# Optimization experiments

Hardware: AMD Instinct MI355X
Metric: run time of the kernel (lower is better)

The kernel has to match this reference:

```python
import jax, jax.numpy as jnp
import numpy as np

ALPHA = float(np.exp(-0.1))  # leak factor exp(-dt/tau) with dt/tau = 0.1


def setup_inputs() -> dict:
    key = jax.random.key(0)
    k1, k2 = jax.random.split(key)
    B, T, H, O = 128, 512, 1024, 256
    x = jax.random.normal(k1, (B, T, H), dtype=jnp.float32)
    # xavier_uniform init for (H, O) weight
    limit = float(np.sqrt(6.0 / (H + O)))
    weight_end = jax.random.uniform(k2, (H, O), dtype=jnp.float32,
                                    minval=-limit, maxval=limit)
    return {"x": x, "weight_end": weight_end}


def reference(x, weight_end):
    # x: [B, T, H], weight_end: [H, O]
    h2 = jnp.einsum('bth,ho->bto', x, weight_end)  # [B, T, O]
    B, T, O = h2.shape
    # leaky-integrate scan over first T-1 steps, accumulating softmax(mem)
    h_seq = jnp.swapaxes(h2[:, :T - 1, :], 0, 1)  # [T-1, B, O]

    def step(carry, h_t):
        mem, out = carry
        mem = ALPHA * mem + (1.0 - ALPHA) * h_t
        out = out + jax.nn.softmax(mem, axis=-1)
        return (mem, out), None

    init = (jnp.zeros((B, O), h2.dtype), jnp.zeros((B, O), h2.dtype))
    (_, out), _ = jax.lax.scan(step, init, h_seq)
    return out
```

## Files before the change

### kernel.cpp

```cpp
#include <hip/hip_runtime.h>

#define B_DIM 128
#define T_DIM 512
#define H_DIM 1024
#define O_DIM 256

typedef short bf16x8 __attribute__((ext_vector_type(8)));
typedef float f32x4 __attribute__((ext_vector_type(4)));

__device__ __forceinline__ unsigned short f2bf(float f) {
    union { float f; unsigned u; } v; v.f = f;
    unsigned u = v.u;
    u += 0x7fffu + ((u >> 16) & 1u);
    return (unsigned short)(u >> 16);
}
__device__ __forceinline__ unsigned pk2(float a, float b) {
    return (unsigned)f2bf(a) | ((unsigned)f2bf(b) << 16);
}

__global__ __launch_bounds__(256) void transpose_w(const float* __restrict__ W,
                                                   unsigned short* __restrict__ Wt) {
    __shared__ float tile[32][33];
    int h0 = blockIdx.x * 32;
    int o0 = blockIdx.y * 32;
    int tx = threadIdx.x;
    int ty = threadIdx.y;
#pragma unroll
    for (int j = 0; j < 32; j += 8)
        tile[ty + j][tx] = W[(size_t)(h0 + ty + j) * O_DIM + o0 + tx];
    __syncthreads();
#pragma unroll
    for (int j = 0; j < 32; j += 8)
        Wt[(size_t)(o0 + ty + j) * H_DIM + h0 + tx] = f2bf(tile[tx][ty + j]);
}

__global__ __launch_bounds__(256) void gemm_bf16(const float* __restrict__ x,
                                                 const unsigned short* __restrict__ Wt,
                                                 float* __restrict__ h2) {
    __shared__ __align__(16) unsigned short As[128 * 40];
    __shared__ __align__(16) unsigned short Bs[128 * 40];

    const int tid  = threadIdx.x;
    const int mb   = blockIdx.x >> 1;
    const int nb   = blockIdx.x & 1;
    const int m0   = mb * 128, n0 = nb * 128;
    const int r    = tid >> 1;
    const int hh   = tid & 1;
    const int lane = tid & 63;
    const int wave = tid >> 6;
    const int wm   = wave >> 1, wn = wave & 1;
    const int rowsel = lane & 15, quad = lane >> 4;

    const float* xg = x + (size_t)(m0 + r) * H_DIM + hh * 16;
    const uint4* wg = (const uint4*)(Wt + (size_t)(n0 + r) * H_DIM + hh * 16);
    uint4* awp = (uint4*)&As[r * 40 + hh * 16];
    uint4* bwp = (uint4*)&Bs[r * 40 + hh * 16];

    const unsigned short* afp = &As[(wm * 64 + rowsel) * 40 + quad * 8];
    const unsigned short* bfp = &Bs[(wn * 64 + rowsel) * 40 + quad * 8];

    f32x4 acc[4][4];
#pragma unroll
    for (int i = 0; i < 4; ++i)
#pragma unroll
        for (int j = 0; j < 4; ++j)
            acc[i][j] = (f32x4){0.f, 0.f, 0.f, 0.f};

    for (int k0 = 0; k0 < H_DIM; k0 += 32) {
        const float4* xa = (const float4*)xg;
        float4 a0 = xa[0], a1 = xa[1], a2 = xa[2], a3 = xa[3];
        uint4 wb0 = wg[0], wb1 = wg[1];
        uint4 p0, p1;
        p0.x = pk2(a0.x, a0.y); p0.y = pk2(a0.z, a0.w);
        p0.z = pk2(a1.x, a1.y); p0.w = pk2(a1.z, a1.w);
        p1.x = pk2(a2.x, a2.y); p1.y = pk2(a2.z, a2.w);
        p1.z = pk2(a3.x, a3.y); p1.w = pk2(a3.z, a3.w);
        awp[0] = p0;  awp[1] = p1;
        bwp[0] = wb0; bwp[1] = wb1;
        __syncthreads();

        bf16x8 af[4], bfr[4];
#pragma unroll
        for (int i = 0; i < 4; ++i) {
            af[i]  = *(const bf16x8*)(afp + i * 16 * 40);
            bfr[i] = *(const bf16x8*)(bfp + i * 16 * 40);
        }
#pragma unroll
        for (int i = 0; i < 4; ++i)
#pragma unroll
            for (int j = 0; j < 4; ++j)
                acc[i][j] = __builtin_amdgcn_mfma_f32_16x16x32_bf16(af[i], bfr[j], acc[i][j], 0, 0, 0);
        __syncthreads();

        xg += 32;
        wg += 4;
    }

#pragma unroll
    for (int i = 0; i < 4; ++i) {
#pragma unroll
        for (int j = 0; j < 4; ++j) {
            int gm = m0 + wm * 64 + i * 16 + quad * 4;
            int gn = n0 + wn * 64 + j * 16 + rowsel;
            float* cp = h2 + (size_t)gm * O_DIM + gn;
            cp[0 * O_DIM] = acc[i][j][0];
            cp[1 * O_DIM] = acc[i][j][1];
            cp[2 * O_DIM] = acc[i][j][2];
            cp[3 * O_DIM] = acc[i][j][3];
        }
    }
}

__global__ __launch_bounds__(64) void snn_scan(const float* __restrict__ h2,
                                               float* __restrict__ out) {
    const int b = blockIdx.x >> 3;
    const int c = blockIdx.x & 7;
    const int t_start = c * 64;
    const int t_end   = min(t_start + 64, T_DIM - 1);
    const int s0      = max(0, t_start - 128);
    const int lane    = threadIdx.x;

    const float A   = 0.90483741803595957f;
    const float OMA = 0.09516258196404043f;

    const float4* p = (const float4*)(h2 + (size_t)b * T_DIM * O_DIM) + (size_t)s0 * 64 + lane;
    float4 mem = {0.f, 0.f, 0.f, 0.f};
    float4 acc = {0.f, 0.f, 0.f, 0.f};
    float4 h = *p;
    for (int t = s0; t < t_end; ++t) {
        p += 64;
        float4 hn = *p;
        mem.x = A * mem.x + OMA * h.x;
        mem.y = A * mem.y + OMA * h.y;
        mem.z = A * mem.z + OMA * h.z;
        mem.w = A * mem.w + OMA * h.w;
        if (t >= t_start) {
            float e0 = __expf(mem.x), e1 = __expf(mem.y);
            float e2 = __expf(mem.z), e3 = __expf(mem.w);
            float s = e0 + e1 + e2 + e3;
            s += __shfl_xor(s, 1);
            s += __shfl_xor(s, 2);
            s += __shfl_xor(s, 4);
            s += __shfl_xor(s, 8);
            s += __shfl_xor(s, 16);
            s += __shfl_xor(s, 32);
            float inv = 1.0f / s;
            acc.x += e0 * inv; acc.y += e1 * inv;
            acc.z += e2 * inv; acc.w += e3 * inv;
        }
        h = hn;
    }
    float* op = out + b * O_DIM + lane * 4;
    atomicAdd(op + 0, acc.x);
    atomicAdd(op + 1, acc.y);
    atomicAdd(op + 2, acc.z);
    atomicAdd(op + 3, acc.w);
}

extern "C" void kernel_launch(void* const* d_in, const int* in_sizes, int n_in,
                              void* d_out, int out_size, void* d_ws, size_t ws_size,
                              hipStream_t stream) {
    const float* x = (const float*)d_in[0];
    const float* W = (const float*)d_in[1];
    float* out = (float*)d_out;

    float* h2 = (float*)d_ws;
    unsigned short* Wt = (unsigned short*)((char*)d_ws +
                         (size_t)B_DIM * T_DIM * O_DIM * sizeof(float));

    hipMemsetAsync(d_out, 0, (size_t)B_DIM * O_DIM * sizeof(float), stream);
    transpose_w<<<dim3(H_DIM / 32, O_DIM / 32), dim3(32, 8), 0, stream>>>(W, Wt);
    gemm_bf16<<<dim3((B_DIM * T_DIM / 128) * 2), 256, 0, stream>>>(x, Wt, h2);
    snn_scan<<<dim3(B_DIM * 8), 64, 0, stream>>>(h2, out);
}
```

Before: 479.8 us.

## Store h2 in bf16, async-load W to LDS, truncate x, shorten scan warmup

The GEMM now writes its intermediate h2 in bf16 rather than fp32, which halves the traffic for both the GEMM store and the scan read. It also loads the weight tile into LDS with global_load_lds in a new layout, and converts x to bf16 by truncation via a byte permute instead of round-to-nearest. The scan warmup drops from 128 to 64 steps and the loop is unrolled by four with prefetched loads. These changes reduce precision in several places: bf16 h2, truncated inputs and a shorter leaky warmup (alpha^64 ≈ 0.0017 residual), so accuracy may suffer.

```diff
diff --git a/kernel.cpp b/kernel.cpp
--- a/kernel.cpp
+++ b/kernel.cpp
@@ -14,8 +14,16 @@
     u += 0x7fffu + ((u >> 16) & 1u);
     return (unsigned short)(u >> 16);
 }
-__device__ __forceinline__ unsigned pk2(float a, float b) {
-    return (unsigned)f2bf(a) | ((unsigned)f2bf(b) << 16);
+
+__device__ __forceinline__ unsigned tpk(float a, float b) {
+    union { float f; unsigned u; } x{a}, y{b};
+    return __builtin_amdgcn_perm(y.u, x.u, 0x07060302u);
+}
+
+__device__ __forceinline__ void async16(const void* g, void* l) {
+    __builtin_amdgcn_global_load_lds(
+        (const __attribute__((address_space(1))) unsigned int*)g,
+        (__attribute__((address_space(3))) unsigned int*)l, 16, 0, 0);
 }
 
 __global__ __launch_bounds__(256) void transpose_w(const float* __restrict__ W,
@@ -36,9 +44,9 @@
 
 __global__ __launch_bounds__(256) void gemm_bf16(const float* __restrict__ x,
                                                  const unsigned short* __restrict__ Wt,
-                                                 float* __restrict__ h2) {
+                                                 unsigned short* __restrict__ h2) {
     __shared__ __align__(16) unsigned short As[128 * 40];
-    __shared__ __align__(16) unsigned short Bs[128 * 40];
+    __shared__ __align__(16) unsigned short Bs[4 * 128 * 8];
 
     const int tid  = threadIdx.x;
     const int mb   = blockIdx.x >> 1;
@@ -52,12 +60,15 @@
     const int rowsel = lane & 15, quad = lane >> 4;
 
     const float* xg = x + (size_t)(m0 + r) * H_DIM + hh * 16;
-    const uint4* wg = (const uint4*)(Wt + (size_t)(n0 + r) * H_DIM + hh * 16);
     uint4* awp = (uint4*)&As[r * 40 + hh * 16];
-    uint4* bwp = (uint4*)&Bs[r * 40 + hh * 16];
+
+    const unsigned short* wg0 = Wt + (size_t)(n0 + lane) * H_DIM + wave * 8;
+    const unsigned short* wg1 = wg0 + (size_t)64 * H_DIM;
+    unsigned short* bs0 = &Bs[wave * 1024];
+    unsigned short* bs1 = &Bs[wave * 1024 + 512];
 
     const unsigned short* afp = &As[(wm * 64 + rowsel) * 40 + quad * 8];
-    const unsigned short* bfp = &Bs[(wn * 64 + rowsel) * 40 + quad * 8];
+    const unsigned short* bfp = &Bs[quad * 1024 + (wn * 64 + rowsel) * 8];
 
     f32x4 acc[4][4];
 #pragma unroll
@@ -67,23 +78,24 @@
             acc[i][j] = (f32x4){0.f, 0.f, 0.f, 0.f};
 
     for (int k0 = 0; k0 < H_DIM; k0 += 32) {
+        async16(wg0, bs0);
+        async16(wg1, bs1);
+
         const float4* xa = (const float4*)xg;
         float4 a0 = xa[0], a1 = xa[1], a2 = xa[2], a3 = xa[3];
-        uint4 wb0 = wg[0], wb1 = wg[1];
         uint4 p0, p1;
-        p0.x = pk2(a0.x, a0.y); p0.y = pk2(a0.z, a0.w);
-        p0.z = pk2(a1.x, a1.y); p0.w = pk2(a1.z, a1.w);
-        p1.x = pk2(a2.x, a2.y); p1.y = pk2(a2.z, a2.w);
-        p1.z = pk2(a3.x, a3.y); p1.w = pk2(a3.z, a3.w);
+        p0.x = tpk(a0.x, a0.y); p0.y = tpk(a0.z, a0.w);
+        p0.z = tpk(a1.x, a1.y); p0.w = tpk(a1.z, a1.w);
+        p1.x = tpk(a2.x, a2.y); p1.y = tpk(a2.z, a2.w);
+        p1.z = tpk(a3.x, a3.y); p1.w = tpk(a3.z, a3.w);
         awp[0] = p0;  awp[1] = p1;
-        bwp[0] = wb0; bwp[1] = wb1;
         __syncthreads();
 
         bf16x8 af[4], bfr[4];
 #pragma unroll
         for (int i = 0; i < 4; ++i) {
             af[i]  = *(const bf16x8*)(afp + i * 16 * 40);
-            bfr[i] = *(const bf16x8*)(bfp + i * 16 * 40);
+            bfr[i] = *(const bf16x8*)(bfp + i * 16 * 8);
         }
 #pragma unroll
         for (int i = 0; i < 4; ++i)
@@ -93,7 +105,8 @@
         __syncthreads();
 
         xg += 32;
-        wg += 4;
+        wg0 += 32;
+        wg1 += 32;
     }
 
 #pragma unroll
@@ -102,54 +115,71 @@
         for (int j = 0; j < 4; ++j) {
             int gm = m0 + wm * 64 + i * 16 + quad * 4;
             int gn = n0 + wn * 64 + j * 16 + rowsel;
-            float* cp = h2 + (size_t)gm * O_DIM + gn;
-            cp[0 * O_DIM] = acc[i][j][0];
-            cp[1 * O_DIM] = acc[i][j][1];
-            cp[2 * O_DIM] = acc[i][j][2];
-            cp[3 * O_DIM] = acc[i][j][3];
+            unsigned short* cp = h2 + (size_t)gm * O_DIM + gn;
+            cp[0 * O_DIM] = f2bf(acc[i][j][0]);
+            cp[1 * O_DIM] = f2bf(acc[i][j][1]);
+            cp[2 * O_DIM] = f2bf(acc[i][j][2]);
+            cp[3 * O_DIM] = f2bf(acc[i][j][3]);
         }
     }
 }
 
-__global__ __launch_bounds__(64) void snn_scan(const float* __restrict__ h2,
+__global__ __launch_bounds__(64) void snn_scan(const unsigned short* __restrict__ h2,
                                                float* __restrict__ out) {
     const int b = blockIdx.x >> 3;
     const int c = blockIdx.x & 7;
     const int t_start = c * 64;
     const int t_end   = min(t_start + 64, T_DIM - 1);
-    const int s0      = max(0, t_start - 128);
+    const int s0      = max(0, t_start - 64);
     const int lane    = threadIdx.x;
 
     const float A   = 0.90483741803595957f;
     const float OMA = 0.09516258196404043f;
 
-    const float4* p = (const float4*)(h2 + (size_t)b * T_DIM * O_DIM) + (size_t)s0 * 64 + lane;
+    const unsigned short* base = h2 + (size_t)b * T_DIM * O_DIM + lane * 4;
+#define LD(row) (*(const uint2*)(base + (size_t)(row) * O_DIM))
+
     float4 mem = {0.f, 0.f, 0.f, 0.f};
     float4 acc = {0.f, 0.f, 0.f, 0.f};
-    float4 h = *p;
-    for (int t = s0; t < t_end; ++t) {
-        p += 64;
-        float4 hn = *p;
-        mem.x = A * mem.x + OMA * h.x;
-        mem.y = A * mem.y + OMA * h.y;
-        mem.z = A * mem.z + OMA * h.z;
-        mem.w = A * mem.w + OMA * h.w;
-        if (t >= t_start) {
-            float e0 = __expf(mem.x), e1 = __expf(mem.y);
-            float e2 = __expf(mem.z), e3 = __expf(mem.w);
-            float s = e0 + e1 + e2 + e3;
-            s += __shfl_xor(s, 1);
-            s += __shfl_xor(s, 2);
-            s += __shfl_xor(s, 4);
-            s += __shfl_xor(s, 8);
-            s += __shfl_xor(s, 16);
-            s += __shfl_xor(s, 32);
-            float inv = 1.0f / s;
-            acc.x += e0 * inv; acc.y += e1 * inv;
-            acc.z += e2 * inv; acc.w += e3 * inv;
-        }
-        h = hn;
-    }
+
+    uint2 u0 = LD(s0), u1 = LD(s0 + 1), u2 = LD(s0 + 2), u3 = LD(s0 + 3);
+
+    const int nIter = (t_end - s0 + 3) & ~3;
+
+#define STEP(U, T)                                                              \
+    {                                                                           \
+        union { unsigned u; float f; } l0, h0, l1, h1;                          \
+        l0.u = (U).x << 16; h0.u = (U).x & 0xffff0000u;                         \
+        l1.u = (U).y << 16; h1.u = (U).y & 0xffff0000u;                         \
+        mem.x = A * mem.x + OMA * l0.f;                                         \
+        mem.y = A * mem.y + OMA * h0.f;                                         \
+        mem.z = A * mem.z + OMA * l1.f;                                         \
+        mem.w = A * mem.w + OMA * h1.f;                                         \
+        if ((T) >= t_start && (T) < t_end) {                                    \
+            float e0 = __expf(mem.x), e1 = __expf(mem.y);                       \
+            float e2 = __expf(mem.z), e3 = __expf(mem.w);                       \
+            float s = e0 + e1 + e2 + e3;                                        \
+            s += __shfl_xor(s, 1);                                              \
+            s += __shfl_xor(s, 2);                                              \
+            s += __shfl_xor(s, 4);                                              \
+            s += __shfl_xor(s, 8);                                              \
+            s += __shfl_xor(s, 16);                                             \
+            s += __shfl_xor(s, 32);                                             \
+            float inv = 1.0f / s;                                               \
+            acc.x += e0 * inv; acc.y += e1 * inv;                               \
+            acc.z += e2 * inv; acc.w += e3 * inv;                               \
+        }                                                                       \
+    }
+
+    for (int t = s0; t < s0 + nIter; t += 4) {
+        STEP(u0, t);     u0 = LD(min(t + 4, T_DIM - 1));
+        STEP(u1, t + 1); u1 = LD(min(t + 5, T_DIM - 1));
+        STEP(u2, t + 2); u2 = LD(min(t + 6, T_DIM - 1));
+        STEP(u3, t + 3); u3 = LD(min(t + 7, T_DIM - 1));
+    }
+#undef STEP
+#undef LD
+
     float* op = out + b * O_DIM + lane * 4;
     atomicAdd(op + 0, acc.x);
     atomicAdd(op + 1, acc.y);
@@ -164,9 +194,9 @@
     const float* W = (const float*)d_in[1];
     float* out = (float*)d_out;
 
-    float* h2 = (float*)d_ws;
+    unsigned short* h2 = (unsigned short*)d_ws;
     unsigned short* Wt = (unsigned short*)((char*)d_ws +
-                         (size_t)B_DIM * T_DIM * O_DIM * sizeof(float));
+                         (size_t)B_DIM * T_DIM * O_DIM * sizeof(unsigned short));
 
     hipMemsetAsync(d_out, 0, (size_t)B_DIM * O_DIM * sizeof(float), stream);
     transpose_w<<<dim3(H_DIM / 32, O_DIM / 32), dim3(32, 8), 0, stream>>>(W, Wt);
```

Measured after the change: 464.9 us. 1.03x faster.
